# Performance work log

Hardware: AMD Instinct MI355X
Metric: run time of the kernel (lower is better)

## Reference

```python
import jax, jax.numpy as jnp
import numpy as np

WINDOW = 2  # window_size

def _causal_window_conv(x, W, b):
    # x: [B,T,D_in], W: [WINDOW, D_in, D_out], b: [D_out]
    # equivalent to left-padding x by WINDOW-1 zeros and a 'valid' conv
    B, T, _ = x.shape
    xp = jnp.pad(x, ((0, 0), (WINDOW - 1, 0), (0, 0)))  # [B, T+WINDOW-1, D_in]
    out = b
    for k in range(WINDOW):
        out = out + jnp.einsum('btd,de->bte', xp[:, k:k + T], W[k])
    return out  # [B,T,D_out]

def setup_inputs() -> dict:
    key = jax.random.key(0)
    ks = jax.random.split(key, 4)
    B, T, Din, Dout = 8, 4096, 256, 256
    scale = 0.05
    x = jax.random.normal(ks[0], (B, T, Din), dtype=jnp.float32)
    W_z = jax.random.normal(ks[1], (WINDOW, Din, Dout), dtype=jnp.float32) * scale
    W_f = jax.random.normal(ks[2], (WINDOW, Din, Dout), dtype=jnp.float32) * scale
    W_o = jax.random.normal(ks[3], (WINDOW, Din, Dout), dtype=jnp.float32) * scale
    b_z = jnp.zeros((Dout,), dtype=jnp.float32)
    b_f = jnp.zeros((Dout,), dtype=jnp.float32)
    b_o = jnp.zeros((Dout,), dtype=jnp.float32)
    return {"x": x, "W_z": W_z, "W_f": W_f, "W_o": W_o,
            "b_z": b_z, "b_f": b_f, "b_o": b_o}

def reference(x, W_z, W_f, W_o, b_z, b_f, b_o):
    # QRNN with fo-pooling (Bradbury et al. 2016), return_sequences=True
    z = jnp.tanh(_causal_window_conv(x, W_z, b_z))          # [B,T,D]
    f = jax.nn.sigmoid(_causal_window_conv(x, W_f, b_f))    # [B,T,D]
    o = jax.nn.sigmoid(_causal_window_conv(x, W_o, b_o))    # [B,T,D]

    def step(c, zfo):
        z_t, f_t, o_t = zfo
        c = f_t * c + (1.0 - f_t) * z_t   # fo-pooling recurrence
        h = o_t * c
        return c, h

    c0 = jnp.zeros(z.shape[::2], dtype=z.dtype)  # [B,D]
    # time-major for scan
    zfo = (z.transpose(1, 0, 2), f.transpose(1, 0, 2), o.transpose(1, 0, 2))
    _, hs = jax.lax.scan(step, c0, zfo)
    return hs.transpose(1, 0, 2)  # [B,T,D]
```

## Files before the change

kernel.cpp:

```cpp
#include <hip/hip_runtime.h>
#include <hip/hip_bf16.h>
#include <hip/hip_fp16.h>

#define BDIM 8
#define TDIM 4096
#define DDIM 256
#define MDIM (BDIM * TDIM)
#define NCHUNK 256
#define LCHUNK (TDIM / NCHUNK)

typedef _Float16 f16x8 __attribute__((ext_vector_type(8)));
typedef _Float16 f16x4 __attribute__((ext_vector_type(4)));
typedef float f32x4 __attribute__((ext_vector_type(4)));

__device__ __forceinline__ float sigmoid_(float x) {
    return 1.0f / (1.0f + __expf(-x));
}
__device__ __forceinline__ float tanh_(float x) {
    return 2.0f / (1.0f + __expf(-2.0f * x)) - 1.0f;
}

#define GLOAD_LDS16(g, l)                                                    \
    __builtin_amdgcn_global_load_lds(                                        \
        (const __attribute__((address_space(1))) void*)(g),                  \
        (__attribute__((address_space(3))) void*)(l), 16, 0, 0)

__global__ __launch_bounds__(256) void prep(
    const float* __restrict__ x, _Float16* __restrict__ xpad,
    const float* __restrict__ Wz, const float* __restrict__ Wf,
    const float* __restrict__ Wo, _Float16* __restrict__ Wt) {
    const int bx = blockIdx.x;
    if (bx < 1536) {
        const int idx = bx * 256 + threadIdx.x;
        const int n = idx & 255;
        const int kin = (idx >> 8) & 255;
        const int w = (idx >> 16) & 1;
        const int g = idx >> 17;
        const float* W = (g == 0) ? Wz : (g == 1) ? Wf : Wo;
        const float v = W[(size_t)w * 65536 + (size_t)kin * 256 + n];
        Wt[((size_t)g * 256 + n) * 512 + w * 256 + kin] = (_Float16)v;
        return;
    }
    const int bxx = bx - 1536;
    const int b = bxx / 1025;
    const int tb = bxx - b * 1025;
    const int tp = tb * 4 + (threadIdx.x >> 6);
    const int q = threadIdx.x & 63;
    if (tp > TDIM) return;
    float4 v = make_float4(0.f, 0.f, 0.f, 0.f);
    if (tp > 0)
        v = *(const float4*)(x + ((size_t)b * TDIM + tp - 1) * DDIM + q * 4);
    f16x4 h;
    h[0] = (_Float16)v.x; h[1] = (_Float16)v.y;
    h[2] = (_Float16)v.z; h[3] = (_Float16)v.w;
    *(f16x4*)(xpad + ((size_t)b * (TDIM + 1) + tp) * DDIM + q * 4) = h;
}

__global__ __launch_bounds__(256, 2) void gates_mfma(
    const _Float16* __restrict__ xpad, const _Float16* __restrict__ Wt,
    const float* __restrict__ bz, const float* __restrict__ bfv,
    const float* __restrict__ bo,
    _Float16* __restrict__ zbuf, _Float16* __restrict__ fbuf,
    _Float16* __restrict__ obuf) {
    const int hw = blockIdx.x;
    const int logical = (hw & 7) * 192 + (hw >> 3);
    const int mblk = logical / 6;
    const int rem = logical - mblk * 6;
    const int gate = rem % 3;
    const int nblk = rem / 3;
    const int m0 = mblk * 128;
    const int n0 = nblk * 128;

    const int tid = threadIdx.x;
    const int lane = tid & 63;
    const int wave = tid >> 6;
    const int wr = wave >> 1;
    const int wc = wave & 1;

    __shared__ __align__(16) char smem[65536];

    const int s = wave * 64 + lane;
    const int r1 = s >> 3;
    const int kc = (((s & 7) ^ ((s >> 3) & 7))) * 8;

    const int b = m0 >> 12;
    const int t0 = m0 & (TDIM - 1);

    const _Float16* srcA =
        xpad + ((size_t)b * (TDIM + 1) + t0 + r1) * DDIM + kc;
    const _Float16* srcB = Wt + ((size_t)gate * 256 + n0 + r1) * 512 + kc;

#define STAGE_(slot, kt)                                                     \
    {                                                                        \
        char* dA = smem + (slot) * 32768 + wave * 1024;                      \
        char* dB = smem + (slot) * 32768 + 16384 + wave * 1024;              \
        GLOAD_LDS16(srcA + (kt) * 64, dA);                                   \
        GLOAD_LDS16(srcA + (kt) * 64 + 32 * DDIM, dA + 4096);                \
        GLOAD_LDS16(srcA + (kt) * 64 + 64 * DDIM, dA + 8192);                \
        GLOAD_LDS16(srcA + (kt) * 64 + 96 * DDIM, dA + 12288);               \
        GLOAD_LDS16(srcB + (kt) * 64, dB);                                   \
        GLOAD_LDS16(srcB + (kt) * 64 + 32 * 512, dB + 4096);                 \
        GLOAD_LDS16(srcB + (kt) * 64 + 64 * 512, dB + 8192);                 \
        GLOAD_LDS16(srcB + (kt) * 64 + 96 * 512, dB + 12288);               \
    }

    f32x4 acc[4][4] = {};
    const int am = lane & 15;
    const int c0 = (((lane >> 4) ^ (lane & 7))) * 8;
    const int c1 = (((4 + (lane >> 4)) ^ (lane & 7))) * 8;

    STAGE_(0, 0);

#pragma unroll
    for (int t = 0; t < 8; ++t) {
        asm volatile("s_waitcnt vmcnt(0)" ::: "memory");
        __builtin_amdgcn_s_barrier();
        __builtin_amdgcn_sched_barrier(0);
        if (t < 7) STAGE_((t + 1) & 1, t + 1);

        const _Float16* Ab = (const _Float16*)(smem + (t & 1) * 32768);
        const _Float16* Bb = Ab + 8192;

        f16x8 a0[4], b0[4], a1[4], b1[4];
#pragma unroll
        for (int i = 0; i < 4; ++i)
            a0[i] = *(const f16x8*)(Ab + (wr * 64 + i * 16 + am) * 64 + c0);
#pragma unroll
        for (int j = 0; j < 4; ++j)
            b0[j] = *(const f16x8*)(Bb + (wc * 64 + j * 16 + am) * 64 + c0);
        __builtin_amdgcn_sched_barrier(0);
#pragma unroll
        for (int i = 0; i < 4; ++i)
            a1[i] = *(const f16x8*)(Ab + (wr * 64 + i * 16 + am) * 64 + c1);
#pragma unroll
        for (int j = 0; j < 4; ++j)
            b1[j] = *(const f16x8*)(Bb + (wc * 64 + j * 16 + am) * 64 + c1);

        asm volatile("s_waitcnt lgkmcnt(8)" ::: "memory");
        __builtin_amdgcn_sched_barrier(0);
        __builtin_amdgcn_s_setprio(1);
#pragma unroll
        for (int i = 0; i < 4; ++i)
#pragma unroll
            for (int j = 0; j < 4; ++j)
                acc[i][j] = __builtin_amdgcn_mfma_f32_16x16x32_f16(
                    b0[j], a0[i], acc[i][j], 0, 0, 0);
        __builtin_amdgcn_s_setprio(0);
        asm volatile("s_waitcnt lgkmcnt(0)" ::: "memory");
        __builtin_amdgcn_sched_barrier(0);
        __builtin_amdgcn_s_setprio(1);
#pragma unroll
        for (int i = 0; i < 4; ++i)
#pragma unroll
            for (int j = 0; j < 4; ++j)
                acc[i][j] = __builtin_amdgcn_mfma_f32_16x16x32_f16(
                    b1[j], a1[i], acc[i][j], 0, 0, 0);
        __builtin_amdgcn_s_setprio(0);
    }
#undef STAGE_

    const float* bias = (gate == 0) ? bz : (gate == 1) ? bfv : bo;
    _Float16* outp = (gate == 0) ? zbuf : (gate == 1) ? fbuf : obuf;
    const int nq = (lane >> 4) * 4;
#pragma unroll
    for (int i = 0; i < 4; ++i) {
        const size_t gm = (size_t)(m0 + wr * 64 + i * 16 + am);
#pragma unroll
        for (int j = 0; j < 4; ++j) {
            const int gc = n0 + wc * 64 + j * 16 + nq;
            const float4 b4 = *(const float4*)(bias + gc);
            f32x4 v = acc[i][j];
            f16x4 h;
            if (gate == 0) {
                h[0] = (_Float16)tanh_(v[0] + b4.x);
                h[1] = (_Float16)tanh_(v[1] + b4.y);
                h[2] = (_Float16)tanh_(v[2] + b4.z);
                h[3] = (_Float16)tanh_(v[3] + b4.w);
            } else {
                h[0] = (_Float16)sigmoid_(v[0] + b4.x);
                h[1] = (_Float16)sigmoid_(v[1] + b4.y);
                h[2] = (_Float16)sigmoid_(v[2] + b4.z);
                h[3] = (_Float16)sigmoid_(v[3] + b4.w);
            }
            *(f16x4*)(outp + gm * DDIM + gc) = h;
        }
    }
}

__global__ __launch_bounds__(256) void scan_pass1(
    const _Float16* __restrict__ zbuf, const _Float16* __restrict__ fbuf,
    float* __restrict__ aggA, float* __restrict__ aggB) {
    const int idx = blockIdx.x * 256 + threadIdx.x;
    const int d4 = idx & 63;
    const int chunk = (idx >> 6) & (NCHUNK - 1);
    const int b = idx >> 14;

    const size_t row0 = (size_t)b * TDIM + (size_t)chunk * LCHUNK;
    const int2* zp = (const int2*)zbuf + row0 * 64 + d4;
    const int2* fp = (const int2*)fbuf + row0 * 64 + d4;

    int2 zr[LCHUNK], fr[LCHUNK];
#pragma unroll
    for (int i = 0; i < LCHUNK; ++i) {
        fr[i] = fp[(size_t)i * 64];
        zr[i] = zp[(size_t)i * 64];
    }

    float A[4], c[4];
#pragma unroll
    for (int e = 0; e < 4; ++e) { A[e] = 1.0f; c[e] = 0.0f; }

#pragma unroll
    for (int i = 0; i < LCHUNK; ++i) {
        const _Float16* fh = (const _Float16*)&fr[i];
        const _Float16* zh = (const _Float16*)&zr[i];
#pragma unroll
        for (int e = 0; e < 4; ++e) {
            const float f = (float)fh[e];
            const float z = (float)zh[e];
            A[e] *= f;
            c[e] = f * c[e] + (1.0f - f) * z;
        }
    }
    ((float4*)aggA)[idx] = make_float4(A[0], A[1], A[2], A[3]);
    ((float4*)aggB)[idx] = make_float4(c[0], c[1], c[2], c[3]);
}

__global__ __launch_bounds__(256) void carry_scan(
    const float* __restrict__ aggA, const float* __restrict__ aggB,
    float* __restrict__ carry) {
    const int g = blockIdx.x * 256 + threadIdx.x;
    const int d = g & 255;
    const int b = g >> 8;
    const size_t base = (size_t)b * NCHUNK * 256 + d;

    float c = 0.0f;
    for (int ch0 = 0; ch0 < NCHUNK; ch0 += 16) {
        float A[16], Bv[16];
#pragma unroll
        for (int u = 0; u < 16; ++u) {
            const size_t p = base + (size_t)(ch0 + u) * 256;
            A[u] = aggA[p];
            Bv[u] = aggB[p];
        }
#pragma unroll
        for (int u = 0; u < 16; ++u) {
            const size_t p = base + (size_t)(ch0 + u) * 256;
            carry[p] = c;
            c = A[u] * c + Bv[u];
        }
    }
}

__global__ __launch_bounds__(256) void scan_pass2(
    const _Float16* __restrict__ zbuf, const _Float16* __restrict__ fbuf,
    const _Float16* __restrict__ obuf, const float* __restrict__ carry,
    float* __restrict__ out) {
    const int idx = blockIdx.x * 256 + threadIdx.x;
    const int d4 = idx & 63;
    const int chunk = (idx >> 6) & (NCHUNK - 1);
    const int b = idx >> 14;

    const size_t row0 = (size_t)b * TDIM + (size_t)chunk * LCHUNK;
    const int2* zp = (const int2*)zbuf + row0 * 64 + d4;
    const int2* fp = (const int2*)fbuf + row0 * 64 + d4;
    const int2* op = (const int2*)obuf + row0 * 64 + d4;
    float4* hp = (float4*)out + row0 * 64 + d4;

    const float4 c0 = ((const float4*)carry)[idx];

    int2 zr[LCHUNK], fr[LCHUNK], orr[LCHUNK];
#pragma unroll
    for (int i = 0; i < LCHUNK; ++i) {
        fr[i] = fp[(size_t)i * 64];
        zr[i] = zp[(size_t)i * 64];
        orr[i] = op[(size_t)i * 64];
    }

    float c[4];
    c[0] = c0.x; c[1] = c0.y; c[2] = c0.z; c[3] = c0.w;

#pragma unroll
    for (int i = 0; i < LCHUNK; ++i) {
        const _Float16* fh = (const _Float16*)&fr[i];
        const _Float16* zh = (const _Float16*)&zr[i];
        const _Float16* oh = (const _Float16*)&orr[i];
        float h[4];
#pragma unroll
        for (int e = 0; e < 4; ++e) {
            const float f = (float)fh[e];
            const float z = (float)zh[e];
            c[e] = f * c[e] + (1.0f - f) * z;
            h[e] = (float)oh[e] * c[e];
        }
        hp[(size_t)i * 64] = make_float4(h[0], h[1], h[2], h[3]);
    }
}

extern "C" void kernel_launch(void* const* d_in, const int* in_sizes, int n_in,
                              void* d_out, int out_size, void* d_ws,
                              size_t ws_size, hipStream_t stream) {
    const float* x = (const float*)d_in[0];
    const float* Wz = (const float*)d_in[1];
    const float* Wf = (const float*)d_in[2];
    const float* Wo = (const float*)d_in[3];
    const float* bz = (const float*)d_in[4];
    const float* bfv = (const float*)d_in[5];
    const float* bo = (const float*)d_in[6];
    float* out = (float*)d_out;

    char* p = (char*)d_ws;
    _Float16* xpad = (_Float16*)p;  p += (size_t)BDIM * (TDIM + 1) * DDIM * 2;
    _Float16* Wt = (_Float16*)p;    p += (size_t)3 * 256 * 512 * 2;
    _Float16* zbuf = (_Float16*)p;  p += (size_t)MDIM * DDIM * 2;
    _Float16* fbuf = (_Float16*)p;  p += (size_t)MDIM * DDIM * 2;
    _Float16* obuf = (_Float16*)p;  p += (size_t)MDIM * DDIM * 2;
    float* aggA = (float*)p;        p += (size_t)BDIM * NCHUNK * DDIM * 4;
    float* aggB = (float*)p;        p += (size_t)BDIM * NCHUNK * DDIM * 4;
    float* carry = (float*)p;

    prep<<<1536 + 1025 * BDIM, 256, 0, stream>>>(x, xpad, Wz, Wf, Wo, Wt);

    gates_mfma<<<MDIM / 128 * (DDIM / 128) * 3, 256, 0, stream>>>(
        xpad, Wt, bz, bfv, bo, zbuf, fbuf, obuf);

    scan_pass1<<<(BDIM * NCHUNK * 64) / 256, 256, 0, stream>>>(zbuf, fbuf,
                                                               aggA, aggB);
    carry_scan<<<(BDIM * DDIM) / 256, 256, 0, stream>>>(aggA, aggB, carry);
    scan_pass2<<<(BDIM * NCHUNK * 64) / 256, 256, 0, stream>>>(zbuf, fbuf,
                                                               obuf, carry, out);
}
```

Baseline: 161.5 us.

## Fuse three-pass chunked scan into one kernel with wave-shuffle carry propagation

Replaces the three scan kernels (chunk aggregate, sequential carry scan, chunk replay) with a single kernel. Each block owns one batch and one 4-channel group across all 4096 timesteps, and combines chunk aggregates with a warp shuffle scan plus a small shared-memory cross-wave step. The GEMM epilogue now writes z/f/o in a channel-group-major, time-contiguous layout so each thread reads its chunk contiguously. This removes two launches, the aggregate/carry round trips and the second read of z/f. In exchange, the scan grid shrinks to 512 blocks and the output stores become strided writes across time.

```diff
diff --git a/kernel.cpp b/kernel.cpp
--- a/kernel.cpp
+++ b/kernel.cpp
@@ -162,9 +162,10 @@
     const float* bias = (gate == 0) ? bz : (gate == 1) ? bfv : bo;
     _Float16* outp = (gate == 0) ? zbuf : (gate == 1) ? fbuf : obuf;
     const int nq = (lane >> 4) * 4;
+    const int tl0 = t0 + wr * 64;
 #pragma unroll
     for (int i = 0; i < 4; ++i) {
-        const size_t gm = (size_t)(m0 + wr * 64 + i * 16 + am);
+        const int tloc = tl0 + i * 16 + am;
 #pragma unroll
         for (int j = 0; j < 4; ++j) {
             const int gc = n0 + wc * 64 + j * 16 + nq;
@@ -182,34 +183,37 @@
                 h[2] = (_Float16)sigmoid_(v[2] + b4.z);
                 h[3] = (_Float16)sigmoid_(v[3] + b4.w);
             }
-            *(f16x4*)(outp + gm * DDIM + gc) = h;
-        }
-    }
-}
-
-__global__ __launch_bounds__(256) void scan_pass1(
+            *(f16x4*)(outp +
+                      (((size_t)(b * 64 + (gc >> 2))) * TDIM + tloc) * 4) = h;
+        }
+    }
+}
+
+__global__ __launch_bounds__(256) void scan_fused(
     const _Float16* __restrict__ zbuf, const _Float16* __restrict__ fbuf,
-    float* __restrict__ aggA, float* __restrict__ aggB) {
-    const int idx = blockIdx.x * 256 + threadIdx.x;
-    const int d4 = idx & 63;
-    const int chunk = (idx >> 6) & (NCHUNK - 1);
-    const int b = idx >> 14;
-
-    const size_t row0 = (size_t)b * TDIM + (size_t)chunk * LCHUNK;
-    const int2* zp = (const int2*)zbuf + row0 * 64 + d4;
-    const int2* fp = (const int2*)fbuf + row0 * 64 + d4;
-
-    int2 zr[LCHUNK], fr[LCHUNK];
+    const _Float16* __restrict__ obuf, float* __restrict__ out) {
+    const int b = blockIdx.x & 7;
+    const int d4 = blockIdx.x >> 3;
+    const int t = threadIdx.x;
+    const int lane = t & 63;
+    const int wv = t >> 6;
+
+    const size_t cb = ((size_t)(b * 64 + d4)) * TDIM;
+    const int2* zp = (const int2*)zbuf + cb;
+    const int2* fp = (const int2*)fbuf + cb;
+    const int2* op = (const int2*)obuf + cb;
+
+    int2 zr[LCHUNK], fr[LCHUNK], orr[LCHUNK];
 #pragma unroll
     for (int i = 0; i < LCHUNK; ++i) {
-        fr[i] = fp[(size_t)i * 64];
-        zr[i] = zp[(size_t)i * 64];
-    }
-
-    float A[4], c[4];
-#pragma unroll
-    for (int e = 0; e < 4; ++e) { A[e] = 1.0f; c[e] = 0.0f; }
-
+        zr[i] = zp[t * LCHUNK + i];
+        fr[i] = fp[t * LCHUNK + i];
+        orr[i] = op[t * LCHUNK + i];
+    }
+
+    float A[4], Bv[4];
+#pragma unroll
+    for (int e = 0; e < 4; ++e) { A[e] = 1.0f; Bv[e] = 0.0f; }
 #pragma unroll
     for (int i = 0; i < LCHUNK; ++i) {
         const _Float16* fh = (const _Float16*)&fr[i];
@@ -219,67 +223,66 @@
             const float f = (float)fh[e];
             const float z = (float)zh[e];
             A[e] *= f;
-            c[e] = f * c[e] + (1.0f - f) * z;
-        }
-    }
-    ((float4*)aggA)[idx] = make_float4(A[0], A[1], A[2], A[3]);
-    ((float4*)aggB)[idx] = make_float4(c[0], c[1], c[2], c[3]);
-}
-
-__global__ __launch_bounds__(256) void carry_scan(
-    const float* __restrict__ aggA, const float* __restrict__ aggB,
-    float* __restrict__ carry) {
-    const int g = blockIdx.x * 256 + threadIdx.x;
-    const int d = g & 255;
-    const int b = g >> 8;
-    const size_t base = (size_t)b * NCHUNK * 256 + d;
-
-    float c = 0.0f;
-    for (int ch0 = 0; ch0 < NCHUNK; ch0 += 16) {
-        float A[16], Bv[16];
-#pragma unroll
-        for (int u = 0; u < 16; ++u) {
-            const size_t p = base + (size_t)(ch0 + u) * 256;
-            A[u] = aggA[p];
-            Bv[u] = aggB[p];
-        }
-#pragma unroll
-        for (int u = 0; u < 16; ++u) {
-            const size_t p = base + (size_t)(ch0 + u) * 256;
-            carry[p] = c;
-            c = A[u] * c + Bv[u];
-        }
-    }
-}
-
-__global__ __launch_bounds__(256) void scan_pass2(
-    const _Float16* __restrict__ zbuf, const _Float16* __restrict__ fbuf,
-    const _Float16* __restrict__ obuf, const float* __restrict__ carry,
-    float* __restrict__ out) {
-    const int idx = blockIdx.x * 256 + threadIdx.x;
-    const int d4 = idx & 63;
-    const int chunk = (idx >> 6) & (NCHUNK - 1);
-    const int b = idx >> 14;
-
-    const size_t row0 = (size_t)b * TDIM + (size_t)chunk * LCHUNK;
-    const int2* zp = (const int2*)zbuf + row0 * 64 + d4;
-    const int2* fp = (const int2*)fbuf + row0 * 64 + d4;
-    const int2* op = (const int2*)obuf + row0 * 64 + d4;
-    float4* hp = (float4*)out + row0 * 64 + d4;
-
-    const float4 c0 = ((const float4*)carry)[idx];
-
-    int2 zr[LCHUNK], fr[LCHUNK], orr[LCHUNK];
-#pragma unroll
-    for (int i = 0; i < LCHUNK; ++i) {
-        fr[i] = fp[(size_t)i * 64];
-        zr[i] = zp[(size_t)i * 64];
-        orr[i] = op[(size_t)i * 64];
+            Bv[e] = f * Bv[e] + (1.0f - f) * z;
+        }
+    }
+
+    float Ai[4], Bi[4];
+#pragma unroll
+    for (int e = 0; e < 4; ++e) { Ai[e] = A[e]; Bi[e] = Bv[e]; }
+#pragma unroll
+    for (int off = 1; off < 64; off <<= 1) {
+        float Au[4], Bu[4];
+#pragma unroll
+        for (int e = 0; e < 4; ++e) {
+            Au[e] = __shfl_up(Ai[e], off);
+            Bu[e] = __shfl_up(Bi[e], off);
+        }
+        if (lane >= off) {
+#pragma unroll
+            for (int e = 0; e < 4; ++e) {
+                Bi[e] = Ai[e] * Bu[e] + Bi[e];
+                Ai[e] = Ai[e] * Au[e];
+            }
+        }
+    }
+
+    __shared__ float sA[4][4], sB[4][4];
+    if (lane == 63) {
+#pragma unroll
+        for (int e = 0; e < 4; ++e) { sA[wv][e] = Ai[e]; sB[wv][e] = Bi[e]; }
+    }
+    __syncthreads();
+    float Ap[4], Bp[4];
+#pragma unroll
+    for (int e = 0; e < 4; ++e) { Ap[e] = 1.0f; Bp[e] = 0.0f; }
+#pragma unroll
+    for (int w = 0; w < 3; ++w) {
+        if (w < wv) {
+#pragma unroll
+            for (int e = 0; e < 4; ++e) {
+                Bp[e] = sA[w][e] * Bp[e] + sB[w][e];
+                Ap[e] = sA[w][e] * Ap[e];
+            }
+        }
+    }
+
+    float Ae[4], Be[4];
+#pragma unroll
+    for (int e = 0; e < 4; ++e) {
+        Ae[e] = __shfl_up(Ai[e], 1);
+        Be[e] = __shfl_up(Bi[e], 1);
+    }
+    if (lane == 0) {
+#pragma unroll
+        for (int e = 0; e < 4; ++e) { Ae[e] = 1.0f; Be[e] = 0.0f; }
     }
 
     float c[4];
-    c[0] = c0.x; c[1] = c0.y; c[2] = c0.z; c[3] = c0.w;
-
+#pragma unroll
+    for (int e = 0; e < 4; ++e) c[e] = Ae[e] * Bp[e] + Be[e];
+
+    float4* hp = (float4*)out + ((size_t)b * TDIM) * 64 + d4;
 #pragma unroll
     for (int i = 0; i < LCHUNK; ++i) {
         const _Float16* fh = (const _Float16*)&fr[i];
@@ -293,7 +296,7 @@
             c[e] = f * c[e] + (1.0f - f) * z;
             h[e] = (float)oh[e] * c[e];
         }
-        hp[(size_t)i * 64] = make_float4(h[0], h[1], h[2], h[3]);
+        hp[(size_t)(t * LCHUNK + i) * 64] = make_float4(h[0], h[1], h[2], h[3]);
     }
 }
 
@@ -315,18 +318,11 @@
     _Float16* zbuf = (_Float16*)p;  p += (size_t)MDIM * DDIM * 2;
     _Float16* fbuf = (_Float16*)p;  p += (size_t)MDIM * DDIM * 2;
     _Float16* obuf = (_Float16*)p;  p += (size_t)MDIM * DDIM * 2;
-    float* aggA = (float*)p;        p += (size_t)BDIM * NCHUNK * DDIM * 4;
-    float* aggB = (float*)p;        p += (size_t)BDIM * NCHUNK * DDIM * 4;
-    float* carry = (float*)p;
 
     prep<<<1536 + 1025 * BDIM, 256, 0, stream>>>(x, xpad, Wz, Wf, Wo, Wt);
 
     gates_mfma<<<MDIM / 128 * (DDIM / 128) * 3, 256, 0, stream>>>(
         xpad, Wt, bz, bfv, bo, zbuf, fbuf, obuf);
 
-    scan_pass1<<<(BDIM * NCHUNK * 64) / 256, 256, 0, stream>>>(zbuf, fbuf,
-                                                               aggA, aggB);
-    carry_scan<<<(BDIM * DDIM) / 256, 256, 0, stream>>>(aggA, aggB, carry);
-    scan_pass2<<<(BDIM * NCHUNK * 64) / 256, 256, 0, stream>>>(zbuf, fbuf,
-                                                               obuf, carry, out);
-}
+    scan_fused<<<BDIM * 64, 256, 0, stream>>>(zbuf, fbuf, obuf, out);
+}
```

After: 152.5 us. 1.06x faster.
